# Optimization experiments

Measured on AMD Instinct MI355X. Metric: run time of the kernel, lower is better.

The kernel has to match this reference:

```python
import jax, jax.numpy as jnp
import numpy as np

B, T, D, H = 2, 4096, 512, 8
DH = D // H  # dim_head = 64


def setup_inputs() -> dict:
    key = jax.random.key(0)
    ks = jax.random.split(key, 10)
    s = 1.0 / np.sqrt(D)
    x = jax.random.normal(ks[0], (B, T, D), dtype=jnp.float32)
    Wq = jax.random.uniform(ks[1], (D, D), jnp.float32, -s, s)
    Wk = jax.random.uniform(ks[2], (D, D), jnp.float32, -s, s)
    Wv = jax.random.uniform(ks[3], (D, D), jnp.float32, -s, s)
    Wo = jax.random.uniform(ks[4], (D, D), jnp.float32, -s, s)
    bq = jnp.zeros((D,), jnp.float32)
    bk = jnp.zeros((D,), jnp.float32)
    bv = jnp.zeros((D,), jnp.float32)
    bo = jnp.zeros((D,), jnp.float32)
    mask = jax.random.randint(ks[5], (1, 1, T, T), 0, 2).astype(bool)
    return {"x": x, "Wq": Wq, "bq": bq, "Wk": Wk, "bk": bk,
            "Wv": Wv, "bv": bv, "Wo": Wo, "bo": bo, "mask": mask}


def reference(x, Wq, bq, Wk, bk, Wv, bv, Wo, bo, mask):
    # QKV projections (self-attention: Q=K=V=x)
    def split_heads(t):
        return t.reshape(B, T, H, DH).transpose(0, 2, 1, 3)  # (B,H,T,DH)
    Q = split_heads(x @ Wq + bq)
    K = split_heads(x @ Wk + bk)
    V = split_heads(x @ Wv + bv)
    # scaled dot-product attention with additive mask penalty (as in source)
    scores = jnp.einsum('bhqd,bhkd->bhqk', Q, K) / np.sqrt(DH)
    scores = scores + (~mask).astype(scores.dtype) * (-1e9)
    att_w = jax.nn.softmax(scores, axis=-1)
    O = jnp.einsum('bhqk,bhkd->bhqd', att_w, V)
    O = O.transpose(0, 2, 1, 3).reshape(B, T, D)
    return O @ Wo + bo
```

## Files before the change

### kernel.cpp

```cpp
#include <hip/hip_runtime.h>
#include <stdint.h>

#define B_ 2
#define T_ 4096
#define D_ 512
#define H_ 8
#define DH_ 64

typedef __bf16 bf16;
typedef __bf16 bf16x4_t __attribute__((ext_vector_type(4)));
typedef __bf16 bf16x8_t __attribute__((ext_vector_type(8)));
typedef float f32x4 __attribute__((ext_vector_type(4)));
typedef short short4_t __attribute__((ext_vector_type(4)));
typedef uint32_t u32;

static constexpr float QSCALE = 0.18033688011112042f;

__device__ __forceinline__ void async16(void* lds, const void* g) {
  __builtin_amdgcn_global_load_lds(
      (const __attribute__((address_space(1))) void*)g,
      (__attribute__((address_space(3))) void*)lds, 16, 0, 0);
}

__global__ __launch_bounds__(256) void prep_kernel(
    const float* __restrict__ x,
    const float* __restrict__ Wq, const float* __restrict__ Wk,
    const float* __restrict__ Wv, const float* __restrict__ Wo,
    const void* __restrict__ maskp,
    bf16* __restrict__ xb, bf16* __restrict__ WTall, bf16* __restrict__ WoT,
    u32* __restrict__ bmask)
{
  int bid = blockIdx.x;
  int tid = threadIdx.x;
  if (bid < 4096) {
    int idx = bid * 256 + tid;
    const float4* xf = (const float4*)x;
    float4 v = xf[idx];
    bf16x4_t o;
    o[0] = (bf16)v.x; o[1] = (bf16)v.y; o[2] = (bf16)v.z; o[3] = (bf16)v.w;
    ((bf16x4_t*)xb)[idx] = o;
  } else if (bid < 8192) {
    int gid = (bid - 4096) * 256 + tid;
    int sel = gid >> 18;
    int idx = gid & 262143;
    int n = idx >> 9, k = idx & 511;
    if (sel < 3) {
      const float* W = (sel == 0) ? Wq : (sel == 1) ? Wk : Wv;
      float v = W[k * 512 + n];
      if (sel == 0) v *= QSCALE;
      WTall[gid] = (bf16)v;
    } else {
      WoT[idx] = (bf16)Wo[k * 512 + n];
    }
  } else {
    int wid = (bid - 8192) * 256 + tid;
    const uint8_t* m8 = (const uint8_t*)maskp;
    bool u8mode = (__ballot(m8[4 * (tid & 63) + 1] != 0) != 0ull);
    int row = wid >> 7, wcol = wid & 127;
    size_t off = (size_t)row * 4096 + (size_t)wcol * 32;
    u32 w = 0;
    if (u8mode) {
      const uint4* p = (const uint4*)(m8 + off);
      uint4 a = p[0], b = p[1];
      u32 ws[8] = {a.x, a.y, a.z, a.w, b.x, b.y, b.z, b.w};
      #pragma unroll
      for (int j = 0; j < 32; ++j)
        if ((ws[j >> 2] >> ((j & 3) * 8)) & 0xffu) w |= (1u << j);
    } else {
      const uint4* p = (const uint4*)((const u32*)maskp + off);
      #pragma unroll
      for (int q = 0; q < 8; ++q) {
        uint4 a = p[q];
        if (a.x) w |= 1u << (q * 4 + 0);
        if (a.y) w |= 1u << (q * 4 + 1);
        if (a.z) w |= 1u << (q * 4 + 2);
        if (a.w) w |= 1u << (q * 4 + 3);
      }
    }
    bmask[((size_t)(row >> 6) * 64 + (wcol >> 1)) * 128 + (row & 63) * 2 + (wcol & 1)] = w;
  }
}

__global__ __launch_bounds__(256) void qkv_kernel(
    const bf16* __restrict__ xb, const bf16* __restrict__ WTall,
    const float* __restrict__ bq, const float* __restrict__ bk,
    const float* __restrict__ bv,
    bf16* __restrict__ Qb, bf16* __restrict__ Kb, bf16* __restrict__ Vtb)
{
  __shared__ char smem[16384];
  char* smX = smem;
  char* smW = smem + 8192;
  int tid = threadIdx.x;
  int lane = tid & 63, wave = tid >> 6;
  int lo = lane & 15, quad = lane >> 4;
  int wr = wave >> 1, wc = wave & 1;
  int bm = blockIdx.x * 64;
  int bn = blockIdx.y * 64;
  int sel = bn >> 9;
  f32x4 acc[2][2] = {};
  for (int kc = 0; kc < 8; ++kc) {
    __syncthreads();
    for (int s = tid; s < 512; s += 256) {
      int row = s >> 3, slot = s & 7;
      int cg = slot ^ (row & 7) ^ ((row >> 3) & 1);
      async16(smX + s * 16, xb + (size_t)(bm + row) * 512 + kc * 64 + cg * 8);
      async16(smW + s * 16, WTall + (size_t)(bn + row) * 512 + kc * 64 + cg * 8);
    }
    __syncthreads();
    #pragma unroll
    for (int ks = 0; ks < 2; ++ks) {
      bf16x8_t a[2], b[2];
      #pragma unroll
      for (int mt = 0; mt < 2; ++mt) {
        int row = wr * 32 + mt * 16 + lo;
        int ch = (ks * 4 + quad) ^ (row & 7) ^ ((row >> 3) & 1);
        a[mt] = *(const bf16x8_t*)(smX + row * 128 + ch * 16);
      }
      #pragma unroll
      for (int nt = 0; nt < 2; ++nt) {
        int row = wc * 32 + nt * 16 + lo;
        int ch = (ks * 4 + quad) ^ (row & 7) ^ ((row >> 3) & 1);
        b[nt] = *(const bf16x8_t*)(smW + row * 128 + ch * 16);
      }
      if (sel < 2) {
        #pragma unroll
        for (int mt = 0; mt < 2; ++mt)
          #pragma unroll
          for (int nt = 0; nt < 2; ++nt)
            acc[mt][nt] = __builtin_amdgcn_mfma_f32_16x16x32_bf16(
                b[nt], a[mt], acc[mt][nt], 0, 0, 0);
      } else {
        #pragma unroll
        for (int mt = 0; mt < 2; ++mt)
          #pragma unroll
          for (int nt = 0; nt < 2; ++nt)
            acc[mt][nt] = __builtin_amdgcn_mfma_f32_16x16x32_bf16(
                a[mt], b[nt], acc[mt][nt], 0, 0, 0);
      }
    }
  }
  int b_ = bm >> 12;
  if (sel < 2) {
    const float* bias = (sel == 0) ? bq : bk;
    bf16* base = (sel == 0) ? Qb : Kb;
    #pragma unroll
    for (int mt = 0; mt < 2; ++mt) {
      int t = (bm & 4095) + wr * 32 + mt * 16 + lo;
      #pragma unroll
      for (int nt = 0; nt < 2; ++nt) {
        int n0 = (bn + wc * 32 + nt * 16 + quad * 4) & 511;
        int h = n0 >> 6, dh0 = n0 & 63;
        bf16x4_t v;
        #pragma unroll
        for (int r = 0; r < 4; ++r) {
          float bs = bias[n0 + r];
          if (sel == 0) bs *= QSCALE;
          v[r] = (bf16)(acc[mt][nt][r] + bs);
        }
        *(bf16x4_t*)(base + (size_t)(b_ * H_ + h) * T_ * DH_ +
                     (size_t)t * 64 + dh0) = v;
      }
    }
  } else {
    #pragma unroll
    for (int nt = 0; nt < 2; ++nt) {
      int n0 = (bn + wc * 32 + nt * 16 + lo) & 511;
      int h = n0 >> 6, dh = n0 & 63;
      float bs = bv[n0];
      #pragma unroll
      for (int mt = 0; mt < 2; ++mt) {
        int t0 = (bm & 4095) + wr * 32 + mt * 16 + quad * 4;
        bf16x4_t v;
        #pragma unroll
        for (int r = 0; r < 4; ++r) v[r] = (bf16)(acc[mt][nt][r] + bs);
        *(bf16x4_t*)(Vtb + ((size_t)(b_ * H_ + h) * DH_ + dh) * T_ + t0) = v;
      }
    }
  }
}

#define SWZ(r) (((r) & 3) | ((((r) >> 3) & 1) << 2))

__global__ __launch_bounds__(256, 4) void attn_kernel(
    const bf16* __restrict__ Qb, const bf16* __restrict__ Kb,
    const bf16* __restrict__ Vtb, const u32* __restrict__ bm2,
    bf16* __restrict__ Obuf)
{
  __shared__ char smem[17408];
  char* smK = smem;
  char* smV = smem + 8192;
  u32* smM = (u32*)(smem + 16384);
  float* smLa = (float*)(smem + 16896);
  float* smLb = (float*)(smem + 17152);
  int tid = threadIdx.x;
  int lane = tid & 63, wave = tid >> 6;
  int lo = lane & 15, quad = lane >> 4;
  int qh = wave & 1, kh = wave >> 1;
  int blk = blockIdx.x;
  int bh = blk & 15;
  int qt64 = blk >> 4;
  int qbase = qt64 * 64;

  const bf16* Kg = Kb + (size_t)bh * T_ * DH_;
  const bf16* Vg = Vtb + (size_t)bh * DH_ * T_;
  const u32* mg = bm2 + (size_t)qt64 * 8192;

  const bf16* Qg = Qb + ((size_t)bh * T_ + qbase + qh * 32) * DH_;
  bf16x8_t qf[2][2];
  #pragma unroll
  for (int qt = 0; qt < 2; ++qt)
    #pragma unroll
    for (int ks = 0; ks < 2; ++ks)
      qf[qt][ks] = *(const bf16x8_t*)(Qg + (qt * 16 + lo) * 64 + ks * 32 + quad * 8);

  bf16 onev = (lo == 0) ? (bf16)1.0f : (bf16)0.0f;
  bf16x8_t ones8 = {onev, onev, onev, onev, onev, onev, onev, onev};

  f32x4 O[2][4] = {};
  f32x4 Ol[2] = {};

  for (int kc = 0; kc < 64; ++kc) {
    __syncthreads();
    #pragma unroll
    for (int i = 0; i < 2; ++i) {
      int s = tid + i * 256;
      int row = s >> 3, slot = s & 7;
      int cg = slot ^ SWZ(row);
      async16(smK + s * 16, Kg + (size_t)(kc * 64 + row) * 64 + cg * 8);
      async16(smV + s * 16, Vg + (size_t)row * T_ + kc * 64 + cg * 8);
    }
    if (tid < 32) async16((char*)smM + tid * 16, mg + kc * 128 + tid * 4);
    __syncthreads();
    f32x4 St[2][2] = {};
    __builtin_amdgcn_s_setprio(1);
    #pragma unroll
    for (int ks = 0; ks < 2; ++ks)
      #pragma unroll
      for (int kt = 0; kt < 2; ++kt) {
        int krow = kh * 32 + ((lo >> 2) << 3) + kt * 4 + (lo & 3);
        int ch = (ks * 4 + quad) ^ SWZ(krow);
        bf16x8_t kf = *(const bf16x8_t*)(smK + krow * 128 + ch * 16);
        #pragma unroll
        for (int qt = 0; qt < 2; ++qt)
          St[kt][qt] = __builtin_amdgcn_mfma_f32_16x16x32_bf16(
              kf, qf[qt][ks], St[kt][qt], 0, 0, 0);
      }
    __builtin_amdgcn_s_setprio(0);
    bf16x8_t pf8[2];
    #pragma unroll
    for (int qt = 0; qt < 2; ++qt) {
      u32 w = smM[(qh * 32 + qt * 16 + lo) * 2 + kh];
      bf16x8_t t;
      #pragma unroll
      for (int kt = 0; kt < 2; ++kt)
        #pragma unroll
        for (int r = 0; r < 4; ++r) {
          int bit = quad * 8 + kt * 4 + r;
          int mb = ((int)(w << (31 - bit))) >> 31;
          u32 pe = __builtin_bit_cast(u32, __builtin_amdgcn_exp2f(St[kt][qt][r]));
          t[kt * 4 + r] = (bf16)__builtin_bit_cast(float, pe & (u32)mb);
        }
      pf8[qt] = t;
    }
    __builtin_amdgcn_s_setprio(1);
    #pragma unroll
    for (int qt = 0; qt < 2; ++qt)
      Ol[qt] = __builtin_amdgcn_mfma_f32_16x16x32_bf16(
          pf8[qt], ones8, Ol[qt], 0, 0, 0);
    #pragma unroll
    for (int dt = 0; dt < 4; ++dt) {
      int d = dt * 16 + lo;
      int c = (kh * 4 + quad) ^ SWZ(d);
      bf16x8_t vf = *(const bf16x8_t*)(smV + d * 128 + c * 16);
      #pragma unroll
      for (int qt = 0; qt < 2; ++qt)
        O[qt][dt] = __builtin_amdgcn_mfma_f32_16x16x32_bf16(
            pf8[qt], vf, O[qt][dt], 0, 0, 0);
    }
    __builtin_amdgcn_s_setprio(0);
  }
  __syncthreads();
  float* smO = (float*)smem;
  if (lo == 0) {
    float* dst = (kh == 0) ? smLa : smLb;
    #pragma unroll
    for (int qt = 0; qt < 2; ++qt)
      #pragma unroll
      for (int r = 0; r < 4; ++r)
        dst[qh * 32 + qt * 16 + quad * 4 + r] = Ol[qt][r];
  }
  if (kh == 1) {
    #pragma unroll
    for (int qt = 0; qt < 2; ++qt)
      #pragma unroll
      for (int dt = 0; dt < 4; ++dt)
        #pragma unroll
        for (int r = 0; r < 4; ++r)
          smO[(qh * 32 + qt * 16 + quad * 4 + r) * 64 + dt * 16 + lo] = O[qt][dt][r];
  }
  __syncthreads();
  if (kh == 0) {
    bf16* Og = Obuf + ((size_t)bh * T_ + qbase + qh * 32) * DH_;
    #pragma unroll
    for (int qt = 0; qt < 2; ++qt) {
      #pragma unroll
      for (int r = 0; r < 4; ++r) {
        int rl = qt * 16 + quad * 4 + r;
        float inv = 1.0f / (smLa[qh * 32 + rl] + smLb[qh * 32 + rl]);
        #pragma unroll
        for (int dt = 0; dt < 4; ++dt) {
          float o = (O[qt][dt][r] + smO[(qh * 32 + rl) * 64 + dt * 16 + lo]) * inv;
          Og[(size_t)rl * 64 + dt * 16 + lo] = (bf16)o;
        }
      }
    }
  }
}

__global__ __launch_bounds__(256) void proj_kernel(
    const bf16* __restrict__ Obuf, const bf16* __restrict__ WoT,
    const float* __restrict__ bo, float* __restrict__ out)
{
  __shared__ char smem[16384];
  char* smA = smem;
  char* smW = smem + 8192;
  int tid = threadIdx.x;
  int lane = tid & 63, wave = tid >> 6;
  int lo = lane & 15, quad = lane >> 4;
  int wr = wave >> 1, wc = wave & 1;
  int bm = blockIdx.x * 64;
  int bn = blockIdx.y * 64;
  int b_ = bm >> 12, trow = bm & 4095;
  f32x4 acc[2][2] = {};
  for (int kc = 0; kc < 8; ++kc) {
    __syncthreads();
    const bf16* Ag = Obuf + ((size_t)(b_ * H_ + kc) * T_ + trow) * DH_;
    for (int s = tid; s < 512; s += 256) {
      int row = s >> 3, slot = s & 7;
      int cg = slot ^ (row & 7) ^ ((row >> 3) & 1);
      async16(smA + s * 16, Ag + row * 64 + cg * 8);
      async16(smW + s * 16, WoT + (size_t)(bn + row) * 512 + kc * 64 + cg * 8);
    }
    __syncthreads();
    #pragma unroll
    for (int ks = 0; ks < 2; ++ks) {
      bf16x8_t a[2], b[2];
      #pragma unroll
      for (int mt = 0; mt < 2; ++mt) {
        int row = wr * 32 + mt * 16 + lo;
        int ch = (ks * 4 + quad) ^ (row & 7) ^ ((row >> 3) & 1);
        a[mt] = *(const bf16x8_t*)(smA + row * 128 + ch * 16);
      }
      #pragma unroll
      for (int nt = 0; nt < 2; ++nt) {
        int row = wc * 32 + nt * 16 + lo;
        int ch = (ks * 4 + quad) ^ (row & 7) ^ ((row >> 3) & 1);
        b[nt] = *(const bf16x8_t*)(smW + row * 128 + ch * 16);
      }
      #pragma unroll
      for (int mt = 0; mt < 2; ++mt)
        #pragma unroll
        for (int nt = 0; nt < 2; ++nt)
          acc[mt][nt] = __builtin_amdgcn_mfma_f32_16x16x32_bf16(
              b[nt], a[mt], acc[mt][nt], 0, 0, 0);
    }
  }
  #pragma unroll
  for (int mt = 0; mt < 2; ++mt) {
    int t = bm + wr * 32 + mt * 16 + lo;
    #pragma unroll
    for (int nt = 0; nt < 2; ++nt) {
      int c0 = bn + wc * 32 + nt * 16 + quad * 4;
      float4 v;
      v.x = acc[mt][nt][0] + bo[c0 + 0];
      v.y = acc[mt][nt][1] + bo[c0 + 1];
      v.z = acc[mt][nt][2] + bo[c0 + 2];
      v.w = acc[mt][nt][3] + bo[c0 + 3];
      *(float4*)(out + (size_t)t * 512 + c0) = v;
    }
  }
}

extern "C" void kernel_launch(void* const* d_in, const int* in_sizes, int n_in,
                              void* d_out, int out_size, void* d_ws, size_t ws_size,
                              hipStream_t stream) {
  const float* x  = (const float*)d_in[0];
  const float* Wq = (const float*)d_in[1];
  const float* bq = (const float*)d_in[2];
  const float* Wk = (const float*)d_in[3];
  const float* bk = (const float*)d_in[4];
  const float* Wv = (const float*)d_in[5];
  const float* bv = (const float*)d_in[6];
  const float* Wo = (const float*)d_in[7];
  const float* bo = (const float*)d_in[8];
  const void* maskp = d_in[9];
  float* out = (float*)d_out;

  char* w = (char*)d_ws;
  bf16* xb    = (bf16*)(w);
  bf16* WTall = (bf16*)(w + 8388608);
  bf16* WoT   = (bf16*)(w + 9961472);
  bf16* Qb    = (bf16*)(w + 10485760);
  bf16* Kb    = (bf16*)(w + 18874368);
  bf16* Vtb   = (bf16*)(w + 27262976);
  bf16* Obuf  = (bf16*)(w + 35651584);
  u32*  bmask = (u32*)(w + 44040192);

  prep_kernel<<<10240, 256, 0, stream>>>(x, Wq, Wk, Wv, Wo, maskp,
                                         xb, WTall, WoT, bmask);
  qkv_kernel<<<dim3(128, 24), 256, 0, stream>>>(xb, WTall, bq, bk, bv,
                                                Qb, Kb, Vtb);
  attn_kernel<<<1024, 256, 0, stream>>>(Qb, Kb, Vtb, bmask, Obuf);
  proj_kernel<<<dim3(128, 8), 256, 0, stream>>>(Obuf, WoT, bo, out);
}
```

Measured before the change: 266.0 us.

## Double-buffer K/V tiles in attention and enlarge QKV GEMM tiles

The attention kernel now uses two LDS buffers for K/V, prefetching the next chunk while computing the current one, with one barrier per chunk instead of two. Mask words are read straight from global memory into registers rather than staged through LDS. The QKV projection tile grows from 64x64 to 128x128 per block, raising register and LDS reuse and shrinking the grid. The costs are double the LDS in attention, which may lower occupancy, and more accumulator registers in the QKV kernel.

```diff
diff --git a/kernel.cpp b/kernel.cpp
--- a/kernel.cpp
+++ b/kernel.cpp
@@ -87,20 +87,22 @@
     const float* __restrict__ bv,
     bf16* __restrict__ Qb, bf16* __restrict__ Kb, bf16* __restrict__ Vtb)
 {
-  __shared__ char smem[16384];
+  __shared__ char smem[32768];
   char* smX = smem;
-  char* smW = smem + 8192;
+  char* smW = smem + 16384;
   int tid = threadIdx.x;
   int lane = tid & 63, wave = tid >> 6;
   int lo = lane & 15, quad = lane >> 4;
   int wr = wave >> 1, wc = wave & 1;
-  int bm = blockIdx.x * 64;
-  int bn = blockIdx.y * 64;
+  int bm = blockIdx.x * 128;
+  int bn = blockIdx.y * 128;
   int sel = bn >> 9;
-  f32x4 acc[2][2] = {};
+  f32x4 acc[4][4] = {};
   for (int kc = 0; kc < 8; ++kc) {
     __syncthreads();
-    for (int s = tid; s < 512; s += 256) {
+    #pragma unroll
+    for (int i = 0; i < 4; ++i) {
+      int s = tid + i * 256;
       int row = s >> 3, slot = s & 7;
       int cg = slot ^ (row & 7) ^ ((row >> 3) & 1);
       async16(smX + s * 16, xb + (size_t)(bm + row) * 512 + kc * 64 + cg * 8);
@@ -109,31 +111,31 @@
     __syncthreads();
     #pragma unroll
     for (int ks = 0; ks < 2; ++ks) {
-      bf16x8_t a[2], b[2];
-      #pragma unroll
-      for (int mt = 0; mt < 2; ++mt) {
-        int row = wr * 32 + mt * 16 + lo;
+      bf16x8_t a[4], b[4];
+      #pragma unroll
+      for (int mt = 0; mt < 4; ++mt) {
+        int row = wr * 64 + mt * 16 + lo;
         int ch = (ks * 4 + quad) ^ (row & 7) ^ ((row >> 3) & 1);
         a[mt] = *(const bf16x8_t*)(smX + row * 128 + ch * 16);
       }
       #pragma unroll
-      for (int nt = 0; nt < 2; ++nt) {
-        int row = wc * 32 + nt * 16 + lo;
+      for (int nt = 0; nt < 4; ++nt) {
+        int row = wc * 64 + nt * 16 + lo;
         int ch = (ks * 4 + quad) ^ (row & 7) ^ ((row >> 3) & 1);
         b[nt] = *(const bf16x8_t*)(smW + row * 128 + ch * 16);
       }
       if (sel < 2) {
         #pragma unroll
-        for (int mt = 0; mt < 2; ++mt)
+        for (int mt = 0; mt < 4; ++mt)
           #pragma unroll
-          for (int nt = 0; nt < 2; ++nt)
+          for (int nt = 0; nt < 4; ++nt)
             acc[mt][nt] = __builtin_amdgcn_mfma_f32_16x16x32_bf16(
                 b[nt], a[mt], acc[mt][nt], 0, 0, 0);
       } else {
         #pragma unroll
-        for (int mt = 0; mt < 2; ++mt)
+        for (int mt = 0; mt < 4; ++mt)
           #pragma unroll
-          for (int nt = 0; nt < 2; ++nt)
+          for (int nt = 0; nt < 4; ++nt)
             acc[mt][nt] = __builtin_amdgcn_mfma_f32_16x16x32_bf16(
                 a[mt], b[nt], acc[mt][nt], 0, 0, 0);
       }
@@ -144,11 +146,11 @@
     const float* bias = (sel == 0) ? bq : bk;
     bf16* base = (sel == 0) ? Qb : Kb;
     #pragma unroll
-    for (int mt = 0; mt < 2; ++mt) {
-      int t = (bm & 4095) + wr * 32 + mt * 16 + lo;
-      #pragma unroll
-      for (int nt = 0; nt < 2; ++nt) {
-        int n0 = (bn + wc * 32 + nt * 16 + quad * 4) & 511;
+    for (int mt = 0; mt < 4; ++mt) {
+      int t = (bm & 4095) + wr * 64 + mt * 16 + lo;
+      #pragma unroll
+      for (int nt = 0; nt < 4; ++nt) {
+        int n0 = (bn + wc * 64 + nt * 16 + quad * 4) & 511;
         int h = n0 >> 6, dh0 = n0 & 63;
         bf16x4_t v;
         #pragma unroll
@@ -163,13 +165,13 @@
     }
   } else {
     #pragma unroll
-    for (int nt = 0; nt < 2; ++nt) {
-      int n0 = (bn + wc * 32 + nt * 16 + lo) & 511;
+    for (int nt = 0; nt < 4; ++nt) {
+      int n0 = (bn + wc * 64 + nt * 16 + lo) & 511;
       int h = n0 >> 6, dh = n0 & 63;
       float bs = bv[n0];
       #pragma unroll
-      for (int mt = 0; mt < 2; ++mt) {
-        int t0 = (bm & 4095) + wr * 32 + mt * 16 + quad * 4;
+      for (int mt = 0; mt < 4; ++mt) {
+        int t0 = (bm & 4095) + wr * 64 + mt * 16 + quad * 4;
         bf16x4_t v;
         #pragma unroll
         for (int r = 0; r < 4; ++r) v[r] = (bf16)(acc[mt][nt][r] + bs);
@@ -186,12 +188,13 @@
     const bf16* __restrict__ Vtb, const u32* __restrict__ bm2,
     bf16* __restrict__ Obuf)
 {
-  __shared__ char smem[17408];
-  char* smK = smem;
-  char* smV = smem + 8192;
-  u32* smM = (u32*)(smem + 16384);
-  float* smLa = (float*)(smem + 16896);
-  float* smLb = (float*)(smem + 17152);
+  __shared__ char smem[33280];
+  char* smK0 = smem;
+  char* smV0 = smem + 8192;
+  char* smK1 = smem + 16384;
+  char* smV1 = smem + 24576;
+  float* smLa = (float*)(smem + 32768);
+  float* smLb = (float*)(smem + 33024);
   int tid = threadIdx.x;
   int lane = tid & 63, wave = tid >> 6;
   int lo = lane & 15, quad = lane >> 4;
@@ -219,18 +222,20 @@
   f32x4 O[2][4] = {};
   f32x4 Ol[2] = {};
 
-  for (int kc = 0; kc < 64; ++kc) {
-    __syncthreads();
+  auto stage = [&](int kc, char* bK, char* bV) {
     #pragma unroll
     for (int i = 0; i < 2; ++i) {
       int s = tid + i * 256;
       int row = s >> 3, slot = s & 7;
       int cg = slot ^ SWZ(row);
-      async16(smK + s * 16, Kg + (size_t)(kc * 64 + row) * 64 + cg * 8);
-      async16(smV + s * 16, Vg + (size_t)row * T_ + kc * 64 + cg * 8);
-    }
-    if (tid < 32) async16((char*)smM + tid * 16, mg + kc * 128 + tid * 4);
-    __syncthreads();
+      async16(bK + s * 16, Kg + (size_t)(kc * 64 + row) * 64 + cg * 8);
+      async16(bV + s * 16, Vg + (size_t)row * T_ + kc * 64 + cg * 8);
+    }
+  };
+  auto mload = [&](int kc, int qt) -> u32 {
+    return mg[kc * 128 + (qh * 32 + qt * 16 + lo) * 2 + kh];
+  };
+  auto compute = [&](const char* bK, const char* bV, u32 w0, u32 w1) {
     f32x4 St[2][2] = {};
     __builtin_amdgcn_s_setprio(1);
     #pragma unroll
@@ -239,7 +244,7 @@
       for (int kt = 0; kt < 2; ++kt) {
         int krow = kh * 32 + ((lo >> 2) << 3) + kt * 4 + (lo & 3);
         int ch = (ks * 4 + quad) ^ SWZ(krow);
-        bf16x8_t kf = *(const bf16x8_t*)(smK + krow * 128 + ch * 16);
+        bf16x8_t kf = *(const bf16x8_t*)(bK + krow * 128 + ch * 16);
         #pragma unroll
         for (int qt = 0; qt < 2; ++qt)
           St[kt][qt] = __builtin_amdgcn_mfma_f32_16x16x32_bf16(
@@ -249,7 +254,7 @@
     bf16x8_t pf8[2];
     #pragma unroll
     for (int qt = 0; qt < 2; ++qt) {
-      u32 w = smM[(qh * 32 + qt * 16 + lo) * 2 + kh];
+      u32 w = (qt == 0) ? w0 : w1;
       bf16x8_t t;
       #pragma unroll
       for (int kt = 0; kt < 2; ++kt)
@@ -271,14 +276,36 @@
     for (int dt = 0; dt < 4; ++dt) {
       int d = dt * 16 + lo;
       int c = (kh * 4 + quad) ^ SWZ(d);
-      bf16x8_t vf = *(const bf16x8_t*)(smV + d * 128 + c * 16);
+      bf16x8_t vf = *(const bf16x8_t*)(bV + d * 128 + c * 16);
       #pragma unroll
       for (int qt = 0; qt < 2; ++qt)
         O[qt][dt] = __builtin_amdgcn_mfma_f32_16x16x32_bf16(
             pf8[qt], vf, O[qt][dt], 0, 0, 0);
     }
     __builtin_amdgcn_s_setprio(0);
-  }
+  };
+
+  stage(0, smK0, smV0);
+  u32 wA0 = mload(0, 0), wA1 = mload(0, 1);
+  asm volatile("s_waitcnt vmcnt(0)" ::: "memory");
+  __builtin_amdgcn_s_barrier();
+
+  for (int it = 0; it < 32; ++it) {
+    int kcA = 2 * it;
+    stage(kcA + 1, smK1, smV1);
+    u32 wB0 = mload(kcA + 1, 0), wB1 = mload(kcA + 1, 1);
+    compute(smK0, smV0, wA0, wA1);
+    asm volatile("s_waitcnt vmcnt(0)" ::: "memory");
+    __builtin_amdgcn_s_barrier();
+    if (it < 31) {
+      stage(kcA + 2, smK0, smV0);
+      wA0 = mload(kcA + 2, 0); wA1 = mload(kcA + 2, 1);
+    }
+    compute(smK1, smV1, wB0, wB1);
+    asm volatile("s_waitcnt vmcnt(0)" ::: "memory");
+    __builtin_amdgcn_s_barrier();
+  }
+
   __syncthreads();
   float* smO = (float*)smem;
   if (lo == 0) {
@@ -408,8 +435,8 @@
 
   prep_kernel<<<10240, 256, 0, stream>>>(x, Wq, Wk, Wv, Wo, maskp,
                                          xb, WTall, WoT, bmask);
-  qkv_kernel<<<dim3(128, 24), 256, 0, stream>>>(xb, WTall, bq, bk, bv,
-                                                Qb, Kb, Vtb);
+  qkv_kernel<<<dim3(64, 12), 256, 0, stream>>>(xb, WTall, bq, bk, bv,
+                                               Qb, Kb, Vtb);
   attn_kernel<<<1024, 256, 0, stream>>>(Qb, Kb, Vtb, bmask, Obuf);
   proj_kernel<<<dim3(128, 8), 256, 0, stream>>>(Obuf, WoT, bo, out);
 }
```

Measured after the change: 276.3 us. 1.04x slower.

## Enlarge QKV tiles and stage epilogue writes through LDS for coalesced stores

Applied to the files above, without the earlier changes.

The QKV GEMM block tile grows from 64x64 to 128x128, so each wave computes a 4x4 MFMA tile and the grid shrinks to 64x12, which increases operand reuse per LDS load. The QKV, attention and projection epilogues now write results into a swizzled LDS tile first and then issue wide, coalesced 16-byte global stores, replacing the scattered 8-byte and 2-byte writes. This costs extra LDS (attention shared memory grows to 25.6KB), extra barriers, and fewer blocks in the QKV launch, which may lower occupancy.

```diff
diff --git a/kernel.cpp b/kernel.cpp
--- a/kernel.cpp
+++ b/kernel.cpp
@@ -87,20 +87,22 @@
     const float* __restrict__ bv,
     bf16* __restrict__ Qb, bf16* __restrict__ Kb, bf16* __restrict__ Vtb)
 {
-  __shared__ char smem[16384];
+  __shared__ char smem[32768];
   char* smX = smem;
-  char* smW = smem + 8192;
+  char* smW = smem + 16384;
   int tid = threadIdx.x;
   int lane = tid & 63, wave = tid >> 6;
   int lo = lane & 15, quad = lane >> 4;
   int wr = wave >> 1, wc = wave & 1;
-  int bm = blockIdx.x * 64;
-  int bn = blockIdx.y * 64;
+  int bm = blockIdx.x * 128;
+  int bn = blockIdx.y * 128;
   int sel = bn >> 9;
-  f32x4 acc[2][2] = {};
+  f32x4 acc[4][4] = {};
   for (int kc = 0; kc < 8; ++kc) {
     __syncthreads();
-    for (int s = tid; s < 512; s += 256) {
+    #pragma unroll
+    for (int i = 0; i < 4; ++i) {
+      int s = tid + i * 256;
       int row = s >> 3, slot = s & 7;
       int cg = slot ^ (row & 7) ^ ((row >> 3) & 1);
       async16(smX + s * 16, xb + (size_t)(bm + row) * 512 + kc * 64 + cg * 8);
@@ -109,72 +111,98 @@
     __syncthreads();
     #pragma unroll
     for (int ks = 0; ks < 2; ++ks) {
-      bf16x8_t a[2], b[2];
-      #pragma unroll
-      for (int mt = 0; mt < 2; ++mt) {
-        int row = wr * 32 + mt * 16 + lo;
+      bf16x8_t a[4], b[4];
+      #pragma unroll
+      for (int mt = 0; mt < 4; ++mt) {
+        int row = wr * 64 + mt * 16 + lo;
         int ch = (ks * 4 + quad) ^ (row & 7) ^ ((row >> 3) & 1);
         a[mt] = *(const bf16x8_t*)(smX + row * 128 + ch * 16);
       }
       #pragma unroll
-      for (int nt = 0; nt < 2; ++nt) {
-        int row = wc * 32 + nt * 16 + lo;
+      for (int nt = 0; nt < 4; ++nt) {
+        int row = wc * 64 + nt * 16 + lo;
         int ch = (ks * 4 + quad) ^ (row & 7) ^ ((row >> 3) & 1);
         b[nt] = *(const bf16x8_t*)(smW + row * 128 + ch * 16);
       }
       if (sel < 2) {
         #pragma unroll
-        for (int mt = 0; mt < 2; ++mt)
+        for (int mt = 0; mt < 4; ++mt)
           #pragma unroll
-          for (int nt = 0; nt < 2; ++nt)
+          for (int nt = 0; nt < 4; ++nt)
             acc[mt][nt] = __builtin_amdgcn_mfma_f32_16x16x32_bf16(
                 b[nt], a[mt], acc[mt][nt], 0, 0, 0);
       } else {
         #pragma unroll
-        for (int mt = 0; mt < 2; ++mt)
+        for (int mt = 0; mt < 4; ++mt)
           #pragma unroll
-          for (int nt = 0; nt < 2; ++nt)
+          for (int nt = 0; nt < 4; ++nt)
             acc[mt][nt] = __builtin_amdgcn_mfma_f32_16x16x32_bf16(
                 a[mt], b[nt], acc[mt][nt], 0, 0, 0);
       }
     }
   }
   int b_ = bm >> 12;
+  __syncthreads();
+  char* smT = smem;
   if (sel < 2) {
     const float* bias = (sel == 0) ? bq : bk;
     bf16* base = (sel == 0) ? Qb : Kb;
     #pragma unroll
-    for (int mt = 0; mt < 2; ++mt) {
-      int t = (bm & 4095) + wr * 32 + mt * 16 + lo;
-      #pragma unroll
-      for (int nt = 0; nt < 2; ++nt) {
-        int n0 = (bn + wc * 32 + nt * 16 + quad * 4) & 511;
-        int h = n0 >> 6, dh0 = n0 & 63;
+    for (int mt = 0; mt < 4; ++mt) {
+      int tl = wr * 64 + mt * 16 + lo;
+      #pragma unroll
+      for (int nt = 0; nt < 4; ++nt) {
+        int c0 = wc * 64 + nt * 16 + quad * 4;
         bf16x4_t v;
         #pragma unroll
         for (int r = 0; r < 4; ++r) {
-          float bs = bias[n0 + r];
+          float bs = bias[(bn & 511) + c0 + r];
           if (sel == 0) bs *= QSCALE;
           v[r] = (bf16)(acc[mt][nt][r] + bs);
         }
-        *(bf16x4_t*)(base + (size_t)(b_ * H_ + h) * T_ * DH_ +
-                     (size_t)t * 64 + dh0) = v;
-      }
+        int chunk = (c0 >> 3) ^ (tl & 15);
+        int half = (c0 >> 2) & 1;
+        *(bf16x4_t*)(smT + tl * 256 + chunk * 16 + half * 8) = v;
+      }
+    }
+    __syncthreads();
+    #pragma unroll
+    for (int it = 0; it < 8; ++it) {
+      int i = tid + it * 256;
+      int tl = i >> 4, c = i & 15;
+      bf16x8_t v = *(const bf16x8_t*)(smT + tl * 256 + ((c ^ (tl & 15)) * 16));
+      int colg = (bn & 511) + c * 8;
+      int h = colg >> 6, dh0 = colg & 63;
+      int t = (bm & 4095) + tl;
+      *(bf16x8_t*)(base + (size_t)(b_ * H_ + h) * T_ * DH_ +
+                   (size_t)t * 64 + dh0) = v;
     }
   } else {
     #pragma unroll
-    for (int nt = 0; nt < 2; ++nt) {
-      int n0 = (bn + wc * 32 + nt * 16 + lo) & 511;
-      int h = n0 >> 6, dh = n0 & 63;
-      float bs = bv[n0];
-      #pragma unroll
-      for (int mt = 0; mt < 2; ++mt) {
-        int t0 = (bm & 4095) + wr * 32 + mt * 16 + quad * 4;
+    for (int nt = 0; nt < 4; ++nt) {
+      int dhl = wc * 64 + nt * 16 + lo;
+      float bs = bv[(bn & 511) + dhl];
+      #pragma unroll
+      for (int mt = 0; mt < 4; ++mt) {
+        int t0 = wr * 64 + mt * 16 + quad * 4;
         bf16x4_t v;
         #pragma unroll
         for (int r = 0; r < 4; ++r) v[r] = (bf16)(acc[mt][nt][r] + bs);
-        *(bf16x4_t*)(Vtb + ((size_t)(b_ * H_ + h) * DH_ + dh) * T_ + t0) = v;
-      }
+        int chunk = (t0 >> 3) ^ (dhl & 15);
+        int half = (t0 >> 2) & 1;
+        *(bf16x4_t*)(smT + dhl * 256 + chunk * 16 + half * 8) = v;
+      }
+    }
+    __syncthreads();
+    #pragma unroll
+    for (int it = 0; it < 8; ++it) {
+      int i = tid + it * 256;
+      int dhl = i >> 4, c = i & 15;
+      bf16x8_t v = *(const bf16x8_t*)(smT + dhl * 256 + ((c ^ (dhl & 15)) * 16));
+      int colg = (bn & 511) + dhl;
+      int h = colg >> 6, dh = colg & 63;
+      int t = (bm & 4095) + c * 8;
+      *(bf16x8_t*)(Vtb + ((size_t)(b_ * H_ + h) * DH_ + dh) * T_ + t) = v;
     }
   }
 }
@@ -186,12 +214,13 @@
     const bf16* __restrict__ Vtb, const u32* __restrict__ bm2,
     bf16* __restrict__ Obuf)
 {
-  __shared__ char smem[17408];
+  __shared__ char smem[25600];
   char* smK = smem;
   char* smV = smem + 8192;
   u32* smM = (u32*)(smem + 16384);
   float* smLa = (float*)(smem + 16896);
   float* smLb = (float*)(smem + 17152);
+  bf16* smOut = (bf16*)(smem + 17408);
   int tid = threadIdx.x;
   int lane = tid & 63, wave = tid >> 6;
   int lo = lane & 15, quad = lane >> 4;
@@ -300,7 +329,6 @@
   }
   __syncthreads();
   if (kh == 0) {
-    bf16* Og = Obuf + ((size_t)bh * T_ + qbase + qh * 32) * DH_;
     #pragma unroll
     for (int qt = 0; qt < 2; ++qt) {
       #pragma unroll
@@ -310,9 +338,18 @@
         #pragma unroll
         for (int dt = 0; dt < 4; ++dt) {
           float o = (O[qt][dt][r] + smO[(qh * 32 + rl) * 64 + dt * 16 + lo]) * inv;
-          Og[(size_t)rl * 64 + dt * 16 + lo] = (bf16)o;
+          smOut[(qh * 32 + rl) * 64 + dt * 16 + lo] = (bf16)o;
         }
       }
+    }
+  }
+  __syncthreads();
+  {
+    bf16* Og = Obuf + ((size_t)bh * T_ + qbase) * DH_;
+    #pragma unroll
+    for (int it = 0; it < 2; ++it) {
+      int i = tid + it * 256;
+      *(bf16x8_t*)(Og + i * 8) = *(const bf16x8_t*)(smOut + i * 8);
     }
   }
 }
@@ -365,19 +402,28 @@
               b[nt], a[mt], acc[mt][nt], 0, 0, 0);
     }
   }
+  __syncthreads();
+  char* smT = smem;
   #pragma unroll
   for (int mt = 0; mt < 2; ++mt) {
-    int t = bm + wr * 32 + mt * 16 + lo;
+    int tl = wr * 32 + mt * 16 + lo;
     #pragma unroll
     for (int nt = 0; nt < 2; ++nt) {
-      int c0 = bn + wc * 32 + nt * 16 + quad * 4;
-      float4 v;
-      v.x = acc[mt][nt][0] + bo[c0 + 0];
-      v.y = acc[mt][nt][1] + bo[c0 + 1];
-      v.z = acc[mt][nt][2] + bo[c0 + 2];
-      v.w = acc[mt][nt][3] + bo[c0 + 3];
-      *(float4*)(out + (size_t)t * 512 + c0) = v;
-    }
+      int c0 = wc * 32 + nt * 16 + quad * 4;
+      f32x4 v;
+      #pragma unroll
+      for (int r = 0; r < 4; ++r) v[r] = acc[mt][nt][r] + bo[bn + c0 + r];
+      int chunk = (c0 >> 2) ^ (tl & 15);
+      *(f32x4*)(smT + tl * 256 + chunk * 16) = v;
+    }
+  }
+  __syncthreads();
+  #pragma unroll
+  for (int it = 0; it < 4; ++it) {
+    int i = tid + it * 256;
+    int tl = i >> 4, c = i & 15;
+    f32x4 v = *(const f32x4*)(smT + tl * 256 + ((c ^ (tl & 15)) * 16));
+    *(f32x4*)(out + (size_t)(bm + tl) * 512 + bn + c * 4) = v;
   }
 }
 
@@ -408,8 +454,8 @@
 
   prep_kernel<<<10240, 256, 0, stream>>>(x, Wq, Wk, Wv, Wo, maskp,
                                          xb, WTall, WoT, bmask);
-  qkv_kernel<<<dim3(128, 24), 256, 0, stream>>>(xb, WTall, bq, bk, bv,
-                                                Qb, Kb, Vtb);
+  qkv_kernel<<<dim3(64, 12), 256, 0, stream>>>(xb, WTall, bq, bk, bv,
+                                               Qb, Kb, Vtb);
   attn_kernel<<<1024, 256, 0, stream>>>(Qb, Kb, Vtb, bmask, Obuf);
   proj_kernel<<<dim3(128, 8), 256, 0, stream>>>(Obuf, WoT, bo, out);
 }
```

New measurement: 268.1 us. About the same (+0.8%).
